# Kernel tuning notes

Hardware: AMD Instinct MI355X
Metric: run time of the kernel (lower is better)

## Reference

```python
import jax, jax.numpy as jnp
import numpy as np

N, E, T, CIN, COUT = 20000, 160000, 8, 64, 128


def setup_inputs() -> dict:
    key = jax.random.key(0)
    ks = jax.random.split(key, 8)
    x = jax.random.normal(ks[0], (T, N, CIN), jnp.float32)
    edge_index = jax.random.randint(ks[1], (2, E), 0, N)
    edge_weight = jax.random.normal(ks[2], (E,), jnp.float32)
    # temporal Conv1d: kernel 3, xavier-ish small init (gain=0.1 in source)
    tconv_w = jax.random.normal(ks[3], (COUT, CIN, 3), jnp.float32) * 0.02
    tconv_b = jnp.zeros((COUT,), jnp.float32)
    ln_g = jnp.ones((COUT,), jnp.float32)
    ln_b = jnp.zeros((COUT,), jnp.float32)
    # residual 1x1 Conv1d (in != out channels)
    res_w = jax.random.normal(ks[4], (COUT, CIN), jnp.float32) * 0.05
    res_b = jnp.zeros((COUT,), jnp.float32)
    # GCNConv linear weight [out, in] and bias
    gcn_w = jax.random.normal(ks[5], (COUT, COUT), jnp.float32) * 0.05
    gcn_b = jnp.zeros((COUT,), jnp.float32)
    return dict(x=x, edge_index=edge_index, edge_weight=edge_weight,
                tconv_w=tconv_w, tconv_b=tconv_b, ln_g=ln_g, ln_b=ln_b,
                res_w=res_w, res_b=res_b, gcn_w=gcn_w, gcn_b=gcn_b)


def reference(x, edge_index, edge_weight, tconv_w, tconv_b, ln_g, ln_b,
              res_w, res_b, gcn_w, gcn_b):
    Tn, Nn, _ = x.shape
    xc = jnp.transpose(x, (1, 2, 0))  # [N, Cin, T]
    # temporal conv over T (kernel 3, pad 1)
    h = jax.lax.conv_general_dilated(
        xc, tconv_w, window_strides=(1,), padding=[(1, 1)],
        dimension_numbers=('NCH', 'OIH', 'NCH')) + tconv_b[None, :, None]
    h = jnp.transpose(h, (0, 2, 1))  # [N, T, Cout]
    # LayerNorm over channel dim
    mu = h.mean(-1, keepdims=True)
    var = ((h - mu) ** 2).mean(-1, keepdims=True)
    h = (h - mu) * jax.lax.rsqrt(var + 1e-5) * ln_g + ln_b
    h = jax.nn.relu(h)
    # 1x1 residual conv: [N,Cin,T] x [Cout,Cin] -> [N,T,Cout]
    res = jnp.einsum('nct,oc->nto', xc, res_w) + res_b
    xcmb = h + res  # [N, T, Cout]
    # --- GCNConv (PyG): softmax edge weights, self-loops, sym-normalize ---
    ew = jax.nn.softmax(edge_weight)  # softmax over all edges (dim=0)
    row, col = edge_index[0], edge_index[1]
    sl = jnp.arange(Nn)
    row_f = jnp.concatenate([row, sl])
    col_f = jnp.concatenate([col, sl])
    w_f = jnp.concatenate([ew, jnp.ones((Nn,), ew.dtype)])  # self-loop weight 1
    deg = jax.ops.segment_sum(w_f, col_f, num_segments=Nn)
    dinv = jnp.where(deg > 0, jax.lax.rsqrt(jnp.maximum(deg, 1e-12)), 0.0)
    norm = dinv[row_f] * w_f * dinv[col_f]  # [E+N]
    xt = jnp.einsum('ntc,oc->nto', xcmb, gcn_w)  # linear transform, all T at once
    msg = norm[:, None, None] * xt[row_f]        # gather sources: [E+N, T, Cout]
    agg = jax.ops.segment_sum(msg, col_f, num_segments=Nn) + gcn_b
    out = jax.nn.relu(agg)  # [N, T, Cout]
    return jnp.transpose(out, (1, 0, 2))  # [T, N, Cout] == stacked per-t list
```

## Files before the change

kernel.cpp:

```cpp
#include <hip/hip_runtime.h>
#include <math.h>

#define N_NODES 20000
#define E_EDGES 160000
#define T_STEPS 8
#define C_IN    64
#define C_OUT   128

typedef __bf16 bf16x8 __attribute__((ext_vector_type(8)));
typedef float  f32x4  __attribute__((ext_vector_type(4)));
#define MFMA16(a, b, c) __builtin_amdgcn_mfma_f32_16x16x32_bf16((a), (b), (c), 0, 0, 0)

__device__ __forceinline__ unsigned short f2u(float f) {
  __bf16 b = (__bf16)f;
  return __builtin_bit_cast(unsigned short, b);
}
__device__ __forceinline__ unsigned int pack2(float lo, float hi) {
  return (unsigned int)f2u(lo) | ((unsigned int)f2u(hi) << 16);
}
__device__ __forceinline__ float ulo(unsigned int u) { return __builtin_bit_cast(float, u << 16); }
__device__ __forceinline__ float uhi(unsigned int u) { return __builtin_bit_cast(float, u & 0xffff0000u); }

__device__ __forceinline__ float wredSum(float v) {
#pragma unroll
  for (int d = 32; d > 0; d >>= 1) v += __shfl_xor(v, d, 64);
  return v;
}
__device__ __forceinline__ float wredMax(float v) {
#pragma unroll
  for (int d = 32; d > 0; d >>= 1) v = fmaxf(v, __shfl_xor(v, d, 64));
  return v;
}
__device__ __forceinline__ int wredSumI(int v) {
#pragma unroll
  for (int d = 32; d > 0; d >>= 1) v += __shfl_xor(v, d, 64);
  return v;
}
__device__ __forceinline__ float bredSum(float v, float* sm4) {
  __syncthreads();
  v = wredSum(v);
  const int lane = threadIdx.x & 63, wid = threadIdx.x >> 6;
  if (lane == 0) sm4[wid] = v;
  __syncthreads();
  return sm4[0] + sm4[1] + sm4[2] + sm4[3];
}
__device__ __forceinline__ float bredMax(float v, float* sm4) {
  __syncthreads();
  v = wredMax(v);
  const int lane = threadIdx.x & 63, wid = threadIdx.x >> 6;
  if (lane == 0) sm4[wid] = v;
  __syncthreads();
  return fmaxf(fmaxf(sm4[0], sm4[1]), fmaxf(sm4[2], sm4[3]));
}

__global__ __launch_bounds__(256) void k_pmax(const float* __restrict__ w, float* __restrict__ pm) {
  __shared__ float sm4[4];
  float m = -3.4e38f;
  for (int i = blockIdx.x * 256 + threadIdx.x; i < E_EDGES; i += 256 * 256) m = fmaxf(m, w[i]);
  m = bredMax(m, sm4);
  if (threadIdx.x == 0) pm[blockIdx.x] = m;
}

__global__ __launch_bounds__(256) void k_sumexp(const float* __restrict__ w, const float* __restrict__ pm,
                                                float* __restrict__ ps) {
  __shared__ float sm4[4];
  const float mx = bredMax(pm[threadIdx.x], sm4);
  float s = 0.f;
  for (int i = blockIdx.x * 256 + threadIdx.x; i < E_EDGES; i += 256 * 256) s += expf(w[i] - mx);
  s = bredSum(s, sm4);
  if (threadIdx.x == 0) ps[blockIdx.x] = s;
}

__global__ __launch_bounds__(256) void k_edge(const float* __restrict__ w, const int* __restrict__ ei,
                                              const float* __restrict__ pm, const float* __restrict__ ps,
                                              float* __restrict__ ewv, float* __restrict__ deg,
                                              int* __restrict__ cnt) {
  __shared__ float sm4[4];
  const float mx  = bredMax(pm[threadIdx.x], sm4);
  const float sum = bredSum(ps[threadIdx.x], sm4);
  const int e = blockIdx.x * 256 + threadIdx.x;
  const float v = expf(w[e] - mx) / sum;
  ewv[e] = v;
  const int c = ei[E_EDGES + e];
  atomicAdd(&deg[c], v);
  atomicAdd(&cnt[c], 1);
}

__global__ __launch_bounds__(256) void k_scanA(const int* __restrict__ cnt, const float* __restrict__ deg,
                                               float* __restrict__ dinv, int* __restrict__ csum) {
  __shared__ int sm4[4];
  const int i = blockIdx.x * 256 + threadIdx.x;
  const int v = (i < N_NODES) ? cnt[i] : 0;
  if (i < N_NODES) dinv[i] = rsqrtf(deg[i]);
  int s = wredSumI(v);
  const int lane = threadIdx.x & 63, wid = threadIdx.x >> 6;
  if (lane == 0) sm4[wid] = s;
  __syncthreads();
  if (threadIdx.x == 0) csum[blockIdx.x] = sm4[0] + sm4[1] + sm4[2] + sm4[3];
}

__global__ __launch_bounds__(128) void k_scanB(const int* __restrict__ csum, int* __restrict__ cbase) {
  __shared__ int buf[128];
  const int tid = threadIdx.x;
  const int nchunk = (N_NODES + 255) / 256;
  const int v = (tid < nchunk) ? csum[tid] : 0;
  buf[tid] = v;
  __syncthreads();
#pragma unroll
  for (int d = 1; d < 128; d <<= 1) {
    const int u = (tid >= d) ? buf[tid - d] : 0;
    __syncthreads();
    buf[tid] += u;
    __syncthreads();
  }
  if (tid < nchunk) cbase[tid] = buf[tid] - v;
}

__global__ __launch_bounds__(256) void k_scanC(const int* __restrict__ cnt, const int* __restrict__ cbase,
                                               int* __restrict__ off, int* __restrict__ cursor) {
  __shared__ int wpart[4];
  const int tid = threadIdx.x, lane = tid & 63, wid = tid >> 6;
  const int i = blockIdx.x * 256 + tid;
  const int v = (i < N_NODES) ? cnt[i] : 0;
  int s = v;
#pragma unroll
  for (int d = 1; d < 64; d <<= 1) { const int u = __shfl_up(s, d, 64); if (lane >= d) s += u; }
  if (lane == 63) wpart[wid] = s;
  __syncthreads();
  int add = cbase[blockIdx.x];
#pragma unroll
  for (int wv = 0; wv < 4; ++wv) if (wv < wid) add += wpart[wv];
  if (i < N_NODES) { const int excl = add + (s - v); off[i] = excl; cursor[i] = excl; }
  if (i == N_NODES - 1) off[N_NODES] = E_EDGES;
}

__global__ __launch_bounds__(256) void k_norm_scatter(const int* __restrict__ ei, const float* __restrict__ ewv,
                                                      const float* __restrict__ dinv, int* __restrict__ cursor,
                                                      uint2* __restrict__ srcnrm) {
  const int e = blockIdx.x * 256 + threadIdx.x;
  const int r = ei[e], c = ei[E_EDGES + e];
  const float nm = dinv[r] * ewv[e] * dinv[c];
  const int pos = atomicAdd(&cursor[c], 1);
  srcnrm[pos] = make_uint2((unsigned int)r, __builtin_bit_cast(unsigned int, nm));
}

__global__ __launch_bounds__(256) void k_wprep(const float* __restrict__ tconv_w, const float* __restrict__ res_w,
                                               const float* __restrict__ gcn_w, unsigned int* __restrict__ Bf,
                                               float* __restrict__ deg, int* __restrict__ cnt) {
  const int gid = blockIdx.x * 256 + threadIdx.x;
  if (gid < N_NODES) { deg[gid] = 1.0f; cnt[gid] = 0; }
  float v0, v1;
  if (gid < 12288) {
    const int reg = gid & 3, l = (gid >> 2) & 63, ct = (gid >> 8) & 7, ks = gid >> 11;
    const int o = ct * 16 + (l & 15);
    const int k0 = ks * 32 + ((l >> 4) & 3) * 8 + reg * 2;
    const int c0 = k0 & 63, tap0 = k0 >> 6;
    const int c1 = (k0 + 1) & 63, tap1 = (k0 + 1) >> 6;
    v0 = tconv_w[o * 192 + c0 * 3 + tap0];
    v1 = tconv_w[o * 192 + c1 * 3 + tap1];
  } else if (gid < 16384) {
    const int g = gid - 12288;
    const int reg = g & 3, l = (g >> 2) & 63, ct = (g >> 8) & 7, ks = g >> 11;
    const int o = ct * 16 + (l & 15);
    const int k0 = ks * 32 + ((l >> 4) & 3) * 8 + reg * 2;
    v0 = res_w[o * 64 + k0];
    v1 = res_w[o * 64 + k0 + 1];
  } else {
    const int g = gid - 16384;
    const int reg = g & 3, l = (g >> 2) & 63, ct = (g >> 8) & 7, ks = g >> 11;
    const int o = ct * 16 + (l & 15);
    const int k0 = ks * 32 + ((l >> 4) & 3) * 8 + reg * 2;
    v0 = gcn_w[o * 128 + k0];
    v1 = gcn_w[o * 128 + k0 + 1];
  }
  Bf[gid] = pack2(v0, v1);
}

#define XS_NODE 720
#define XS_SLOT 72
#define AS2_STRIDE 136
__global__ __launch_bounds__(256, 2) void k_fuse(const float* __restrict__ x,
                                                 const float* __restrict__ tconv_b,
                                                 const float* __restrict__ ln_g, const float* __restrict__ ln_b,
                                                 const float* __restrict__ res_b,
                                                 const unsigned int* __restrict__ Bf,
                                                 unsigned short* __restrict__ xt,
                                                 unsigned char* __restrict__ xq,
                                                 float* __restrict__ qsc) {
  const int tid = threadIdx.x, lane = tid & 63, w = tid >> 6;
  const int l15 = lane & 15, lg = lane >> 4;
  const int n0 = blockIdx.x * 16;

  __shared__ __align__(16) unsigned short XsAs[128 * AS2_STRIDE];
  unsigned short* Xs  = XsAs;
  unsigned short* As2 = XsAs;
  __shared__ float psum[4][128], psq[4][128];
  __shared__ float smu[128], srs[128];
  __shared__ unsigned int nmax[16];

  if (tid < 16) nmax[tid] = 0u;

#pragma unroll
  for (int p = 0; p < 8; ++p) {
    const int chunk = p * 256 + tid;
    const int tq = chunk >> 8, nn = (chunk >> 4) & 15, c4 = chunk & 15;
    const float4 v = *(const float4*)(x + ((size_t)tq * N_NODES + n0 + nn) * C_IN + c4 * 4);
    uint2 pk; pk.x = pack2(v.x, v.y); pk.y = pack2(v.z, v.w);
    *(uint2*)&Xs[nn * XS_NODE + (tq + 1) * XS_SLOT + c4 * 4] = pk;
  }
#pragma unroll
  for (int p = 0; p < 3; ++p) {
    const int i = p * 256 + tid;
    if (i < 576) {
      const int nn = i / 36;
      const int r = i - nn * 36;
      const int sl = (r < 18) ? 0 : 9;
      const int of = ((r < 18) ? r : r - 18) * 4;
      *(uint2*)&Xs[nn * XS_NODE + sl * XS_SLOT + of] = make_uint2(0u, 0u);
    }
  }

  const uint4* Bf4 = (const uint4*)Bf;
  uint4 Bc[2][6], Br[2][2];
#pragma unroll
  for (int ct = 0; ct < 2; ++ct) {
    const int ctg = w * 2 + ct;
#pragma unroll
    for (int ks = 0; ks < 6; ++ks) Bc[ct][ks] = Bf4[(ks * 8 + ctg) * 64 + lane];
#pragma unroll
    for (int ks = 0; ks < 2; ++ks) Br[ct][ks] = Bf4[3072 + (ks * 8 + ctg) * 64 + lane];
  }
  float cb[2], rb[2], gv[2], bv[2];
#pragma unroll
  for (int ct = 0; ct < 2; ++ct) {
    const int col = w * 32 + ct * 16 + l15;
    cb[ct] = tconv_b[col]; rb[ct] = res_b[col]; gv[ct] = ln_g[col]; bv[ct] = ln_b[col];
  }
  __syncthreads();

  f32x4 accC[8][2], accR[8][2];
#pragma unroll
  for (int rt = 0; rt < 8; ++rt)
#pragma unroll
    for (int ct = 0; ct < 2; ++ct) { accC[rt][ct] = (f32x4)0.f; accR[rt][ct] = (f32x4)0.f; }

#pragma unroll
  for (int ks = 0; ks < 6; ++ks) {
    bf16x8 af[8];
    const int slot = (l15 & 7) + (ks >> 1);
    const int koff = slot * XS_SLOT + (ks & 1) * 32 + lg * 8;
#pragma unroll
    for (int rt = 0; rt < 8; ++rt) {
      const int node = rt * 2 + (l15 >> 3);
      af[rt] = *(const bf16x8*)&Xs[node * XS_NODE + koff];
    }
#pragma unroll
    for (int rt = 0; rt < 8; ++rt)
#pragma unroll
      for (int ct = 0; ct < 2; ++ct)
        accC[rt][ct] = MFMA16(af[rt], __builtin_bit_cast(bf16x8, Bc[ct][ks]), accC[rt][ct]);
    if (ks == 2 || ks == 3) {
#pragma unroll
      for (int rt = 0; rt < 8; ++rt)
#pragma unroll
        for (int ct = 0; ct < 2; ++ct)
          accR[rt][ct] = MFMA16(af[rt], __builtin_bit_cast(bf16x8, Br[ct][ks - 2]), accR[rt][ct]);
    }
  }

#pragma unroll
  for (int rt = 0; rt < 8; ++rt) {
    float s[4], s2[4];
#pragma unroll
    for (int j = 0; j < 4; ++j) {
      const float h0 = accC[rt][0][j] + cb[0];
      const float h1 = accC[rt][1][j] + cb[1];
      accC[rt][0][j] = h0; accC[rt][1][j] = h1;
      s[j] = h0 + h1; s2[j] = h0 * h0 + h1 * h1;
    }
#pragma unroll
    for (int d = 1; d < 16; d <<= 1)
#pragma unroll
      for (int j = 0; j < 4; ++j) { s[j] += __shfl_xor(s[j], d, 64); s2[j] += __shfl_xor(s2[j], d, 64); }
    if (l15 == 0)
#pragma unroll
      for (int j = 0; j < 4; ++j) {
        psum[w][rt * 16 + lg * 4 + j] = s[j];
        psq[w][rt * 16 + lg * 4 + j] = s2[j];
      }
  }
  __syncthreads();
  if (tid < 128) {
    const float S  = psum[0][tid] + psum[1][tid] + psum[2][tid] + psum[3][tid];
    const float S2 = psq[0][tid] + psq[1][tid] + psq[2][tid] + psq[3][tid];
    const float mu = S * (1.f / 128.f);
    const float var = S2 * (1.f / 128.f) - mu * mu;
    smu[tid] = mu; srs[tid] = rsqrtf(var + 1e-5f);
  }
  __syncthreads();

#pragma unroll
  for (int rt = 0; rt < 8; ++rt)
#pragma unroll
    for (int j = 0; j < 4; ++j) {
      const int row = rt * 16 + lg * 4 + j;
      const float mu = smu[row], rs = srs[row];
      const int sw = ((row >> 3) & 1) << 4;
#pragma unroll
      for (int ct = 0; ct < 2; ++ct) {
        float xc = (accC[rt][ct][j] - mu) * rs * gv[ct] + bv[ct];
        xc = fmaxf(xc, 0.f) + accR[rt][ct][j] + rb[ct];
        const int col = w * 32 + ct * 16 + l15;
        As2[row * AS2_STRIDE + (col ^ sw)] = f2u(xc);
      }
    }
  __syncthreads();

  uint4 Bg[2][4];
#pragma unroll
  for (int ct = 0; ct < 2; ++ct)
#pragma unroll
    for (int ks = 0; ks < 4; ++ks) Bg[ct][ks] = Bf4[4096 + (ks * 8 + (w * 2 + ct)) * 64 + lane];

  f32x4 acc[8][2];
#pragma unroll
  for (int rt = 0; rt < 8; ++rt)
#pragma unroll
    for (int ct = 0; ct < 2; ++ct) acc[rt][ct] = (f32x4)0.f;

  const int swr = ((l15 >> 3) & 1) << 4;
#pragma unroll
  for (int ks = 0; ks < 4; ++ks) {
    bf16x8 af[8];
    const int koff = (ks * 32 + lg * 8) ^ swr;
#pragma unroll
    for (int rt = 0; rt < 8; ++rt)
      af[rt] = *(const bf16x8*)&As2[(rt * 16 + l15) * AS2_STRIDE + koff];
#pragma unroll
    for (int rt = 0; rt < 8; ++rt)
#pragma unroll
      for (int ct = 0; ct < 2; ++ct)
        acc[rt][ct] = MFMA16(af[rt], __builtin_bit_cast(bf16x8, Bg[ct][ks]), acc[rt][ct]);
  }

#pragma unroll
  for (int rt = 0; rt < 8; ++rt) {
    const int nn = rt * 2 + (lg >> 1);
    float m = 0.f;
#pragma unroll
    for (int ct = 0; ct < 2; ++ct)
#pragma unroll
      for (int j = 0; j < 4; ++j) m = fmaxf(m, fabsf(acc[rt][ct][j]));
    atomicMax(&nmax[nn], __builtin_bit_cast(unsigned int, m));
  }
  __syncthreads();
  if (tid < 16) qsc[n0 + tid] = __builtin_bit_cast(float, nmax[tid]) * (1.f / 127.f);

  const int t0 = (lg & 1) * 4;
#pragma unroll
  for (int rt = 0; rt < 8; ++rt) {
    const int nn = rt * 2 + (lg >> 1);
    const size_t n = (size_t)(n0 + nn);
    const float mx = __builtin_bit_cast(float, nmax[nn]);
    const float inv = (mx > 0.f) ? 127.f / mx : 0.f;
#pragma unroll
    for (int ct = 0; ct < 2; ++ct) {
      const int col = w * 32 + ct * 16 + l15;
      uint2 pk;
      pk.x = pack2(acc[rt][ct][0], acc[rt][ct][1]);
      pk.y = pack2(acc[rt][ct][2], acc[rt][ct][3]);
      *(uint2*)(xt + (n * C_OUT + col) * T_STEPS + t0) = pk;
      unsigned int pk8 = 0;
#pragma unroll
      for (int j = 0; j < 4; ++j) {
        const int q = (int)rintf(acc[rt][ct][j] * inv) + 128;
        pk8 |= ((unsigned int)q) << (8 * j);
      }
      *(unsigned int*)(xq + (n * C_OUT + col) * T_STEPS + t0) = pk8;
    }
  }
}

__global__ __launch_bounds__(256) void k_agg(const unsigned short* __restrict__ xt,
                                             const unsigned char* __restrict__ xq,
                                             const float* __restrict__ qsc,
                                             const uint2* __restrict__ srcnrm,
                                             const int* __restrict__ off, const float* __restrict__ dinv,
                                             const float* __restrict__ gcn_b, float* __restrict__ out) {
  const int tid = threadIdx.x, lane = tid & 63, w = tid >> 6;
  const int j = blockIdx.x * 4 + w;
  const int s = off[j], e = off[j + 1];
  const float d2 = dinv[j] * dinv[j];

  float acc[2][8];
#pragma unroll
  for (int h = 0; h < 2; ++h) {
    const uint4 q = *(const uint4*)(xt + ((size_t)j * C_OUT + h * 64 + lane) * T_STEPS);
    acc[h][0] = d2 * ulo(q.x); acc[h][1] = d2 * uhi(q.x);
    acc[h][2] = d2 * ulo(q.y); acc[h][3] = d2 * uhi(q.y);
    acc[h][4] = d2 * ulo(q.z); acc[h][5] = d2 * uhi(q.z);
    acc[h][6] = d2 * ulo(q.w); acc[h][7] = d2 * uhi(q.w);
  }

  float summul = 0.f;
  for (int k = s; k < e; ++k) {
    const uint2 sn = srcnrm[k];
    const int r = (int)sn.x;
    const float mul = __builtin_bit_cast(float, sn.y) * qsc[r];
    summul += mul;
    const uint2 qa = *(const uint2*)(xq + ((size_t)r * C_OUT + lane) * T_STEPS);
    const uint2 qb = *(const uint2*)(xq + ((size_t)r * C_OUT + 64 + lane) * T_STEPS);
#pragma unroll
    for (int tt = 0; tt < 4; ++tt) {
      acc[0][tt]     = fmaf((float)((qa.x >> (8 * tt)) & 0xffu), mul, acc[0][tt]);
      acc[0][4 + tt] = fmaf((float)((qa.y >> (8 * tt)) & 0xffu), mul, acc[0][4 + tt]);
      acc[1][tt]     = fmaf((float)((qb.x >> (8 * tt)) & 0xffu), mul, acc[1][tt]);
      acc[1][4 + tt] = fmaf((float)((qb.y >> (8 * tt)) & 0xffu), mul, acc[1][4 + tt]);
    }
  }

  const float corr = 128.f * summul;
  const float b0 = gcn_b[lane], b1 = gcn_b[64 + lane];
#pragma unroll
  for (int h = 0; h < 2; ++h) {
    const float bo = h ? b1 : b0;
#pragma unroll
    for (int t = 0; t < 8; ++t) {
      const float v = acc[h][t] - corr + bo;
      out[((size_t)t * N_NODES + j) * C_OUT + h * 64 + lane] = fmaxf(v, 0.f);
    }
  }
}

extern "C" void kernel_launch(void* const* d_in, const int* in_sizes, int n_in,
                              void* d_out, int out_size, void* d_ws, size_t ws_size,
                              hipStream_t stream) {
  (void)in_sizes; (void)n_in; (void)out_size; (void)ws_size;
  const float* x       = (const float*)d_in[0];
  const int*   ei      = (const int*)d_in[1];
  const float* ewt     = (const float*)d_in[2];
  const float* tconv_w = (const float*)d_in[3];
  const float* tconv_b = (const float*)d_in[4];
  const float* ln_g    = (const float*)d_in[5];
  const float* ln_b    = (const float*)d_in[6];
  const float* res_w   = (const float*)d_in[7];
  const float* res_b   = (const float*)d_in[8];
  const float* gcn_w   = (const float*)d_in[9];
  const float* gcn_b   = (const float*)d_in[10];
  float* out = (float*)d_out;

  unsigned short* xt = (unsigned short*)d_ws;
  unsigned char*  xq = (unsigned char*)(xt + (size_t)N_NODES * C_OUT * T_STEPS);
  float* qsc  = (float*)(xq + (size_t)N_NODES * C_OUT * T_STEPS);
  unsigned int* Bf = (unsigned int*)(qsc + N_NODES);
  float* ewv   = (float*)(Bf + 24576);
  float* deg   = ewv + E_EDGES;
  float* dinv  = deg + N_NODES;
  float* pm    = dinv + N_NODES;
  float* ps    = pm + 256;
  int*   cnt    = (int*)(ps + 256);
  int*   off    = cnt + N_NODES;
  int*   cursor = off + N_NODES + 1;
  int*   csum   = cursor + N_NODES;
  int*   cbase  = csum + 128;
  uint2* srcnrm = (uint2*)(((size_t)(cbase + 128) + 15) & ~(size_t)15);

  const int nblk = (N_NODES + 255) / 256;
  const int eblk = E_EDGES / 256;

  k_wprep<<<96, 256, 0, stream>>>(tconv_w, res_w, gcn_w, Bf, deg, cnt);
  k_pmax<<<256, 256, 0, stream>>>(ewt, pm);
  k_sumexp<<<256, 256, 0, stream>>>(ewt, pm, ps);
  k_edge<<<eblk, 256, 0, stream>>>(ewt, ei, pm, ps, ewv, deg, cnt);
  k_scanA<<<nblk, 256, 0, stream>>>(cnt, deg, dinv, csum);
  k_scanB<<<1, 128, 0, stream>>>(csum, cbase);
  k_scanC<<<nblk, 256, 0, stream>>>(cnt, cbase, off, cursor);
  k_norm_scatter<<<eblk, 256, 0, stream>>>(ei, ewv, dinv, cursor, srcnrm);

  k_fuse<<<1250, 256, 0, stream>>>(x, tconv_b, ln_g, ln_b, res_b, Bf, xt, xq, qsc);
  k_agg<<<N_NODES / 4, 256, 0, stream>>>(xt, xq, qsc, srcnrm, off, dinv, gcn_b, out);
}
```

Before: 146.3 us.

## Drop bf16 self-loop buffer, merge softmax passes, fold scan into scanC

```diff
diff --git a/kernel.cpp b/kernel.cpp
--- a/kernel.cpp
+++ b/kernel.cpp
@@ -18,8 +18,6 @@
 __device__ __forceinline__ unsigned int pack2(float lo, float hi) {
   return (unsigned int)f2u(lo) | ((unsigned int)f2u(hi) << 16);
 }
-__device__ __forceinline__ float ulo(unsigned int u) { return __builtin_bit_cast(float, u << 16); }
-__device__ __forceinline__ float uhi(unsigned int u) { return __builtin_bit_cast(float, u & 0xffff0000u); }
 
 __device__ __forceinline__ float wredSum(float v) {
 #pragma unroll
@@ -52,23 +50,28 @@
   __syncthreads();
   return fmaxf(fmaxf(sm4[0], sm4[1]), fmaxf(sm4[2], sm4[3]));
 }
-
-__global__ __launch_bounds__(256) void k_pmax(const float* __restrict__ w, float* __restrict__ pm) {
+__device__ __forceinline__ int bredSumI(int v, int* sm4) {
+  __syncthreads();
+  v = wredSumI(v);
+  const int lane = threadIdx.x & 63, wid = threadIdx.x >> 6;
+  if (lane == 0) sm4[wid] = v;
+  __syncthreads();
+  return sm4[0] + sm4[1] + sm4[2] + sm4[3];
+}
+
+__global__ __launch_bounds__(256) void k_esoft(const float* __restrict__ w,
+                                               float* __restrict__ pm, float* __restrict__ ps) {
   __shared__ float sm4[4];
-  float m = -3.4e38f;
-  for (int i = blockIdx.x * 256 + threadIdx.x; i < E_EDGES; i += 256 * 256) m = fmaxf(m, w[i]);
-  m = bredMax(m, sm4);
-  if (threadIdx.x == 0) pm[blockIdx.x] = m;
-}
-
-__global__ __launch_bounds__(256) void k_sumexp(const float* __restrict__ w, const float* __restrict__ pm,
-                                                float* __restrict__ ps) {
-  __shared__ float sm4[4];
-  const float mx = bredMax(pm[threadIdx.x], sm4);
-  float s = 0.f;
-  for (int i = blockIdx.x * 256 + threadIdx.x; i < E_EDGES; i += 256 * 256) s += expf(w[i] - mx);
-  s = bredSum(s, sm4);
-  if (threadIdx.x == 0) ps[blockIdx.x] = s;
+  float m = -3.4e38f, s = 0.f;
+  for (int i = blockIdx.x * 256 + threadIdx.x; i < E_EDGES; i += 256 * 256) {
+    const float xw = w[i];
+    if (xw > m) { s = s * expf(m - xw) + 1.f; m = xw; }
+    else        { s += expf(xw - m); }
+  }
+  const float M = bredMax(m, sm4);
+  const float sp = (s > 0.f) ? s * expf(m - M) : 0.f;
+  const float S = bredSum(sp, sm4);
+  if (threadIdx.x == 0) { pm[blockIdx.x] = M; ps[blockIdx.x] = S; }
 }
 
 __global__ __launch_bounds__(256) void k_edge(const float* __restrict__ w, const int* __restrict__ ei,
@@ -76,8 +79,10 @@
                                               float* __restrict__ ewv, float* __restrict__ deg,
                                               int* __restrict__ cnt) {
   __shared__ float sm4[4];
-  const float mx  = bredMax(pm[threadIdx.x], sm4);
-  const float sum = bredSum(ps[threadIdx.x], sm4);
+  const float mloc = pm[threadIdx.x];
+  const float mx   = bredMax(mloc, sm4);
+  const float sp   = ps[threadIdx.x] * expf(mloc - mx);
+  const float sum  = bredSum(sp, sm4);
   const int e = blockIdx.x * 256 + threadIdx.x;
   const float v = expf(w[e] - mx) / sum;
   ewv[e] = v;
@@ -99,27 +104,14 @@
   if (threadIdx.x == 0) csum[blockIdx.x] = sm4[0] + sm4[1] + sm4[2] + sm4[3];
 }
 
-__global__ __launch_bounds__(128) void k_scanB(const int* __restrict__ csum, int* __restrict__ cbase) {
-  __shared__ int buf[128];
-  const int tid = threadIdx.x;
-  const int nchunk = (N_NODES + 255) / 256;
-  const int v = (tid < nchunk) ? csum[tid] : 0;
-  buf[tid] = v;
-  __syncthreads();
-#pragma unroll
-  for (int d = 1; d < 128; d <<= 1) {
-    const int u = (tid >= d) ? buf[tid - d] : 0;
-    __syncthreads();
-    buf[tid] += u;
-    __syncthreads();
-  }
-  if (tid < nchunk) cbase[tid] = buf[tid] - v;
-}
-
-__global__ __launch_bounds__(256) void k_scanC(const int* __restrict__ cnt, const int* __restrict__ cbase,
+__global__ __launch_bounds__(256) void k_scanC(const int* __restrict__ cnt, const int* __restrict__ csum,
                                                int* __restrict__ off, int* __restrict__ cursor) {
+  __shared__ int smI[4];
   __shared__ int wpart[4];
   const int tid = threadIdx.x, lane = tid & 63, wid = tid >> 6;
+  const int nchunk = (N_NODES + 255) / 256;
+  const int vb = (tid < nchunk && tid < blockIdx.x) ? csum[tid] : 0;
+  const int base = bredSumI(vb, smI);
   const int i = blockIdx.x * 256 + tid;
   const int v = (i < N_NODES) ? cnt[i] : 0;
   int s = v;
@@ -127,7 +119,7 @@
   for (int d = 1; d < 64; d <<= 1) { const int u = __shfl_up(s, d, 64); if (lane >= d) s += u; }
   if (lane == 63) wpart[wid] = s;
   __syncthreads();
-  int add = cbase[blockIdx.x];
+  int add = base;
 #pragma unroll
   for (int wv = 0; wv < 4; ++wv) if (wv < wid) add += wpart[wv];
   if (i < N_NODES) { const int excl = add + (s - v); off[i] = excl; cursor[i] = excl; }
@@ -184,7 +176,6 @@
                                                  const float* __restrict__ ln_g, const float* __restrict__ ln_b,
                                                  const float* __restrict__ res_b,
                                                  const unsigned int* __restrict__ Bf,
-                                                 unsigned short* __restrict__ xt,
                                                  unsigned char* __restrict__ xq,
                                                  float* __restrict__ qsc) {
   const int tid = threadIdx.x, lane = tid & 63, w = tid >> 6;
@@ -366,10 +357,6 @@
 #pragma unroll
     for (int ct = 0; ct < 2; ++ct) {
       const int col = w * 32 + ct * 16 + l15;
-      uint2 pk;
-      pk.x = pack2(acc[rt][ct][0], acc[rt][ct][1]);
-      pk.y = pack2(acc[rt][ct][2], acc[rt][ct][3]);
-      *(uint2*)(xt + (n * C_OUT + col) * T_STEPS + t0) = pk;
       unsigned int pk8 = 0;
 #pragma unroll
       for (int j = 0; j < 4; ++j) {
@@ -381,8 +368,7 @@
   }
 }
 
-__global__ __launch_bounds__(256) void k_agg(const unsigned short* __restrict__ xt,
-                                             const unsigned char* __restrict__ xq,
+__global__ __launch_bounds__(256) void k_agg(const unsigned char* __restrict__ xq,
                                              const float* __restrict__ qsc,
                                              const uint2* __restrict__ srcnrm,
                                              const int* __restrict__ off, const float* __restrict__ dinv,
@@ -394,15 +380,25 @@
 
   float acc[2][8];
 #pragma unroll
-  for (int h = 0; h < 2; ++h) {
-    const uint4 q = *(const uint4*)(xt + ((size_t)j * C_OUT + h * 64 + lane) * T_STEPS);
-    acc[h][0] = d2 * ulo(q.x); acc[h][1] = d2 * uhi(q.x);
-    acc[h][2] = d2 * ulo(q.y); acc[h][3] = d2 * uhi(q.y);
-    acc[h][4] = d2 * ulo(q.z); acc[h][5] = d2 * uhi(q.z);
-    acc[h][6] = d2 * ulo(q.w); acc[h][7] = d2 * uhi(q.w);
-  }
-
-  float summul = 0.f;
+  for (int h = 0; h < 2; ++h)
+#pragma unroll
+    for (int t = 0; t < 8; ++t) acc[h][t] = 0.f;
+
+  float summul;
+  {
+    const float mul = d2 * qsc[j];
+    summul = mul;
+    const uint2 qa = *(const uint2*)(xq + ((size_t)j * C_OUT + lane) * T_STEPS);
+    const uint2 qb = *(const uint2*)(xq + ((size_t)j * C_OUT + 64 + lane) * T_STEPS);
+#pragma unroll
+    for (int tt = 0; tt < 4; ++tt) {
+      acc[0][tt]     = fmaf((float)((qa.x >> (8 * tt)) & 0xffu), mul, acc[0][tt]);
+      acc[0][4 + tt] = fmaf((float)((qa.y >> (8 * tt)) & 0xffu), mul, acc[0][4 + tt]);
+      acc[1][tt]     = fmaf((float)((qb.x >> (8 * tt)) & 0xffu), mul, acc[1][tt]);
+      acc[1][4 + tt] = fmaf((float)((qb.y >> (8 * tt)) & 0xffu), mul, acc[1][4 + tt]);
+    }
+  }
+
   for (int k = s; k < e; ++k) {
     const uint2 sn = srcnrm[k];
     const int r = (int)sn.x;
@@ -449,8 +445,7 @@
   const float* gcn_b   = (const float*)d_in[10];
   float* out = (float*)d_out;
 
-  unsigned short* xt = (unsigned short*)d_ws;
-  unsigned char*  xq = (unsigned char*)(xt + (size_t)N_NODES * C_OUT * T_STEPS);
+  unsigned char* xq = (unsigned char*)d_ws;
   float* qsc  = (float*)(xq + (size_t)N_NODES * C_OUT * T_STEPS);
   unsigned int* Bf = (unsigned int*)(qsc + N_NODES);
   float* ewv   = (float*)(Bf + 24576);
@@ -462,21 +457,18 @@
   int*   off    = cnt + N_NODES;
   int*   cursor = off + N_NODES + 1;
   int*   csum   = cursor + N_NODES;
-  int*   cbase  = csum + 128;
-  uint2* srcnrm = (uint2*)(((size_t)(cbase + 128) + 15) & ~(size_t)15);
+  uint2* srcnrm = (uint2*)(((size_t)(csum + 128) + 15) & ~(size_t)15);
 
   const int nblk = (N_NODES + 255) / 256;
   const int eblk = E_EDGES / 256;
 
   k_wprep<<<96, 256, 0, stream>>>(tconv_w, res_w, gcn_w, Bf, deg, cnt);
-  k_pmax<<<256, 256, 0, stream>>>(ewt, pm);
-  k_sumexp<<<256, 256, 0, stream>>>(ewt, pm, ps);
+  k_esoft<<<256, 256, 0, stream>>>(ewt, pm, ps);
   k_edge<<<eblk, 256, 0, stream>>>(ewt, ei, pm, ps, ewv, deg, cnt);
   k_scanA<<<nblk, 256, 0, stream>>>(cnt, deg, dinv, csum);
-  k_scanB<<<1, 128, 0, stream>>>(csum, cbase);
-  k_scanC<<<nblk, 256, 0, stream>>>(cnt, cbase, off, cursor);
+  k_scanC<<<nblk, 256, 0, stream>>>(cnt, csum, off, cursor);
   k_norm_scatter<<<eblk, 256, 0, stream>>>(ei, ewv, dinv, cursor, srcnrm);
 
-  k_fuse<<<1250, 256, 0, stream>>>(x, tconv_b, ln_g, ln_b, res_b, Bf, xt, xq, qsc);
-  k_agg<<<N_NODES / 4, 256, 0, stream>>>(xt, xq, qsc, srcnrm, off, dinv, gcn_b, out);
-}
+  k_fuse<<<1250, 256, 0, stream>>>(x, tconv_b, ln_g, ln_b, res_b, Bf, xq, qsc);
+  k_agg<<<N_NODES / 4, 256, 0, stream>>>(xq, qsc, srcnrm, off, dinv, gcn_b, out);
+}
```

Result: faster. 135.6 us (-7.3%).
